# Kernel optimization log

Hardware: AMD Instinct MI355X
Metric: run time of the kernel (lower is better)

The kernel has to match this reference:

```python
import jax, jax.numpy as jnp
import numpy as np

N_NODES = 50000
N_EDGES = 600000
IN_DIM = 128
HID = 128
N_CLASSES = 40
N_GRAPHS = 128


def setup_inputs() -> dict:
    key = jax.random.key(0)
    ks = jax.random.split(key, 12)
    x = jax.random.normal(ks[0], (N_NODES, IN_DIM), dtype=jnp.float32)
    edge_index = jax.random.randint(ks[1], (2, N_EDGES), 0, N_NODES, dtype=jnp.int64)
    batch = jnp.sort(jax.random.randint(ks[2], (N_NODES,), 0, N_GRAPHS, dtype=jnp.int64))
    dims = [IN_DIM, HID, HID, N_CLASSES]
    params = {}
    for l in range(3):
        d_in, d_out = dims[l], dims[l + 1]
        s = 1.0 / np.sqrt(d_in)
        params[f"Wl{l}"] = jax.random.uniform(ks[3 + 3 * l], (d_out, d_in), jnp.float32, -s, s)
        params[f"bl{l}"] = jax.random.uniform(ks[4 + 3 * l], (d_out,), jnp.float32, -s, s)
        params[f"Wr{l}"] = jax.random.uniform(ks[5 + 3 * l], (d_out, d_in), jnp.float32, -s, s)
    return {"x": x, "edge_index": edge_index, "batch": batch, **params}


def _sage_layer(h, src, dst, Wl, bl, Wr):
    # message: relu(x_j) (edge_attr is None -> zero), mean-aggregate at dst
    m = jnp.maximum(h[src], 0.0)                       # [E, d]
    agg = jax.ops.segment_sum(m, dst, num_segments=N_NODES)
    cnt = jax.ops.segment_sum(jnp.ones((m.shape[0],), h.dtype), dst, num_segments=N_NODES)
    agg = agg / jnp.maximum(cnt, 1.0)[:, None]
    # lin_l(agg) + lin_r(x)
    return agg @ Wl.T + bl + h @ Wr.T


def reference(x, edge_index, batch, Wl0, bl0, Wr0, Wl1, bl1, Wr1, Wl2, bl2, Wr2):
    src, dst = edge_index[0], edge_index[1]
    Ws = [(Wl0, bl0, Wr0), (Wl1, bl1, Wr1), (Wl2, bl2, Wr2)]
    h = x
    for l, (Wl, bl, Wr) in enumerate(Ws):
        # dropout is identity in eval mode
        h = _sage_layer(h, src, dst, Wl, bl, Wr)
        if l != len(Ws) - 1:
            h = jnp.maximum(h, 0.0)
    # global mean pool over graphs
    gsum = jax.ops.segment_sum(h, batch, num_segments=N_GRAPHS)
    gcnt = jax.ops.segment_sum(jnp.ones((h.shape[0],), h.dtype), batch, num_segments=N_GRAPHS)
    g = gsum / jnp.maximum(gcnt, 1.0)[:, None]
    return h, g
```

## Files before the change

kernel.cpp:

```cpp
#include <hip/hip_runtime.h>
#include <hip/hip_bf16.h>


#define NODES 50000
#define K_DIM 128
#define N_GRAPHS 128

typedef __attribute__((ext_vector_type(8))) short short8;
typedef __attribute__((ext_vector_type(4))) short short4v;
typedef __attribute__((ext_vector_type(4))) float f32x4;

__device__ inline short f2bf(float f) {
    unsigned u = __builtin_bit_cast(unsigned, f);
    u += 0x7FFFu + ((u >> 16) & 1u);
    return (short)(u >> 16);
}
__device__ inline float bf2f(short h) {
    unsigned u = ((unsigned)(unsigned short)h) << 16;
    return __builtin_bit_cast(float, u);
}
__device__ inline float blo(unsigned u) { return __builtin_bit_cast(float, u << 16); }
__device__ inline float bhi(unsigned u) { return __builtin_bit_cast(float, u & 0xFFFF0000u); }
__device__ inline unsigned hilo_pack(float f) {
    short h = f2bf(f);
    short l = f2bf(f - bf2f(h));
    return ((unsigned)(unsigned short)h) | (((unsigned)(unsigned short)l) << 16);
}

__global__ void init_kernel(const float* __restrict__ w0, const float* __restrict__ w1,
                            const float* __restrict__ w2, const float* __restrict__ w3,
                            const float* __restrict__ w4, const float* __restrict__ w5,
                            short* __restrict__ whi, short* __restrict__ wlo,
                            int* __restrict__ deg, const int* __restrict__ batch,
                            int* __restrict__ gstart,
                            const float* __restrict__ x, short* __restrict__ xb,
                            short* __restrict__ xhi, short* __restrict__ xlo, int N) {
    int idx = blockIdx.x * 256 + threadIdx.x;
    if (idx < N * (K_DIM / 4)) {
        float4 v = reinterpret_cast<const float4*>(x)[idx];
        unsigned px = hilo_pack(v.x), py = hilo_pack(v.y);
        unsigned pz = hilo_pack(v.z), pw = hilo_pack(v.w);
        short4v b, hh, ll;
        b[0] = f2bf(fmaxf(v.x, 0.f)); hh[0] = (short)(px & 0xFFFFu); ll[0] = (short)(px >> 16);
        b[1] = f2bf(fmaxf(v.y, 0.f)); hh[1] = (short)(py & 0xFFFFu); ll[1] = (short)(py >> 16);
        b[2] = f2bf(fmaxf(v.z, 0.f)); hh[2] = (short)(pz & 0xFFFFu); ll[2] = (short)(pz >> 16);
        b[3] = f2bf(fmaxf(v.w, 0.f)); hh[3] = (short)(pw & 0xFFFFu); ll[3] = (short)(pw >> 16);
        *reinterpret_cast<short4v*>(&xb [idx * 4]) = b;
        *reinterpret_cast<short4v*>(&xhi[idx * 4]) = hh;
        *reinterpret_cast<short4v*>(&xlo[idx * 4]) = ll;
    }
    if (idx < N) deg[idx] = 0;
    const int TOT = 4 * 16384 + 96 * 128;
    if (idx < TOT) {
        float v;
        if (idx < 65536) {
            int m = idx >> 14, e = idx & 16383;
            const float* W = (m == 0) ? w0 : (m == 1) ? w1 : (m == 2) ? w2 : w3;
            v = W[e];
        } else {
            int i2 = idx - 65536;
            int row = i2 >> 7, col = i2 & 127;
            if (row < 40)      v = w4[row * 128 + col];
            else if (row < 80) v = w5[(row - 40) * 128 + col];
            else               v = 0.f;
        }
        unsigned p = hilo_pack(v);
        whi[idx] = (short)(p & 0xFFFFu);
        wlo[idx] = (short)(p >> 16);
    }
    if (idx <= N_GRAPHS) {
        int g = idx;
        int lo = 0, hi = N;
        while (lo < hi) {
            int mid = (lo + hi) >> 1;
            if (batch[mid] < g) lo = mid + 1; else hi = mid;
        }
        gstart[g] = lo;
    }
}

__global__ void deg_kernel(const int* __restrict__ dst, int* __restrict__ deg, int E) {
    int e = blockIdx.x * blockDim.x + threadIdx.x;
    if (e < E) atomicAdd(&deg[dst[e]], 1);
}

__global__ void scan_p1(const int* __restrict__ deg, int* __restrict__ bsum, int N) {
    int i = blockIdx.x * 256 + threadIdx.x;
    int v = (i < N) ? deg[i] : 0;
    #pragma unroll
    for (int off = 32; off > 0; off >>= 1) v += __shfl_down(v, off, 64);
    __shared__ int ws[4];
    int lane = threadIdx.x & 63, wv = threadIdx.x >> 6;
    if (lane == 0) ws[wv] = v;
    __syncthreads();
    if (threadIdx.x == 0) bsum[blockIdx.x] = ws[0] + ws[1] + ws[2] + ws[3];
}

__global__ void scan_p23(const int* __restrict__ deg, const int* __restrict__ bsum,
                         int* __restrict__ rowptr, int* __restrict__ fillpos,
                         int N, int NB) {
    const int tid = threadIdx.x, lane = tid & 63, wv = tid >> 6;
    __shared__ int ws[4];
    __shared__ int sboff[256];
    {
        int v = (tid < NB) ? bsum[tid] : 0;
        int incl = v;
        #pragma unroll
        for (int off = 1; off < 64; off <<= 1) {
            int t = __shfl_up(incl, off, 64);
            if (lane >= off) incl += t;
        }
        if (lane == 63) ws[wv] = incl;
        __syncthreads();
        int add = 0;
        for (int k = 0; k < wv; ++k) add += ws[k];
        sboff[tid] = incl + add - v;
        __syncthreads();
    }
    const int boff = sboff[blockIdx.x];
    int i = blockIdx.x * 256 + tid;
    int v = (i < N) ? deg[i] : 0;
    int incl = v;
    #pragma unroll
    for (int off = 1; off < 64; off <<= 1) {
        int t = __shfl_up(incl, off, 64);
        if (lane >= off) incl += t;
    }
    __shared__ int ws2[4];
    if (lane == 63) ws2[wv] = incl;
    __syncthreads();
    int add = 0;
    for (int k = 0; k < wv; ++k) add += ws2[k];
    int excl = boff + incl + add - v;
    if (i < N) { rowptr[i] = excl; fillpos[i] = excl; }
    if (i == N) rowptr[N] = excl;
}

__global__ void fill_kernel(const int* __restrict__ src, const int* __restrict__ dst,
                            int* __restrict__ fillpos, int* __restrict__ csr_src, int E) {
    int e = blockIdx.x * blockDim.x + threadIdx.x;
    if (e < E) {
        int p = atomicAdd(&fillpos[dst[e]], 1);
        csr_src[p] = src[e];
    }
}

__global__ void agg_bf16(const unsigned short* __restrict__ hb,
                         const int* __restrict__ rowptr,
                         const int* __restrict__ csr_src,
                         short* __restrict__ aggb, int N) {
    int w = (blockIdx.x * blockDim.x + threadIdx.x) >> 6;
    if (w >= N) return;
    int lane = threadIdx.x & 63;
    int half = lane >> 5, l32 = lane & 31;
    int s = rowptr[w], e = rowptr[w + 1];
    float4 acc = make_float4(0.f, 0.f, 0.f, 0.f);
    int i = s + half;
    for (; i + 6 < e; i += 8) {
        int s0 = csr_src[i], s1 = csr_src[i + 2], s2 = csr_src[i + 4], s3 = csr_src[i + 6];
        uint2 v0 = reinterpret_cast<const uint2*>(hb + (size_t)s0 * K_DIM)[l32];
        uint2 v1 = reinterpret_cast<const uint2*>(hb + (size_t)s1 * K_DIM)[l32];
        uint2 v2 = reinterpret_cast<const uint2*>(hb + (size_t)s2 * K_DIM)[l32];
        uint2 v3 = reinterpret_cast<const uint2*>(hb + (size_t)s3 * K_DIM)[l32];
        acc.x += (blo(v0.x) + blo(v1.x)) + (blo(v2.x) + blo(v3.x));
        acc.y += (bhi(v0.x) + bhi(v1.x)) + (bhi(v2.x) + bhi(v3.x));
        acc.z += (blo(v0.y) + blo(v1.y)) + (blo(v2.y) + blo(v3.y));
        acc.w += (bhi(v0.y) + bhi(v1.y)) + (bhi(v2.y) + bhi(v3.y));
    }
    for (; i < e; i += 2) {
        int s0 = csr_src[i];
        uint2 v0 = reinterpret_cast<const uint2*>(hb + (size_t)s0 * K_DIM)[l32];
        acc.x += blo(v0.x); acc.y += bhi(v0.x);
        acc.z += blo(v0.y); acc.w += bhi(v0.y);
    }
    acc.x += __shfl_xor(acc.x, 32, 64);
    acc.y += __shfl_xor(acc.y, 32, 64);
    acc.z += __shfl_xor(acc.z, 32, 64);
    acc.w += __shfl_xor(acc.w, 32, 64);
    if (half == 0) {
        float inv = 1.0f / fmaxf((float)(e - s), 1.0f);
        short4v b;
        b[0] = f2bf(acc.x * inv);
        b[1] = f2bf(acc.y * inv);
        b[2] = f2bf(acc.z * inv);
        b[3] = f2bf(acc.w * inv);
        *reinterpret_cast<short4v*>(&aggb[(size_t)w * K_DIM + l32 * 4]) = b;
    }
}

__global__ __launch_bounds__(256) void sage_mfma(
        const short* __restrict__ Ab_in,
        const short* __restrict__ Hhi_in, const short* __restrict__ Hlo_in,
        const short* __restrict__ Bhl, const short* __restrict__ Bll,
        const short* __restrict__ Bhr, const short* __restrict__ Blr,
        const float* __restrict__ bl,
        short* __restrict__ outHi, short* __restrict__ outLo, int N) {
    constexpr int BM = 64;
    constexpr int LSTR = 40;
    const int tid = threadIdx.x;
    const int lane = tid & 63;
    const int wave = tid >> 6;
    const int l15 = lane & 15;
    const int quad = lane >> 4;
    const int m0 = blockIdx.x * BM;
    const int srow = tid >> 2, sc8 = tid & 3;

    __shared__ __align__(16) short Ahi[BM * LSTR];
    __shared__ __align__(16) short Alo[BM * LSTR];

    f32x4 acc[4][2];
    #pragma unroll
    for (int i = 0; i < 4; ++i)
        #pragma unroll
        for (int j = 0; j < 2; ++j) acc[i][j] = (f32x4){0.f, 0.f, 0.f, 0.f};

    const short8 zero8 = (short8){0, 0, 0, 0, 0, 0, 0, 0};
    const int sm = m0 + srow;

    for (int k0 = 0; k0 < K_DIM; k0 += 32) {
        __syncthreads();
        {
            short8 v = zero8;
            if (sm < N) v = *reinterpret_cast<const short8*>(Ab_in + (size_t)sm * K_DIM + k0 + sc8 * 8);
            *reinterpret_cast<short8*>(&Ahi[srow * LSTR + sc8 * 8]) = v;
        }
        short8 bh[2], bo[2];
        #pragma unroll
        for (int nt = 0; nt < 2; ++nt) {
            int n = wave * 32 + nt * 16 + l15;
            bh[nt] = *reinterpret_cast<const short8*>(Bhl + (size_t)n * K_DIM + k0 + quad * 8);
            bo[nt] = *reinterpret_cast<const short8*>(Bll + (size_t)n * K_DIM + k0 + quad * 8);
        }
        __syncthreads();
        #pragma unroll
        for (int mt = 0; mt < 4; ++mt) {
            int row = mt * 16 + l15;
            short8 ab = *reinterpret_cast<const short8*>(&Ahi[row * LSTR + quad * 8]);
            #pragma unroll
            for (int nt = 0; nt < 2; ++nt) {
                acc[mt][nt] = __builtin_amdgcn_mfma_f32_16x16x32_bf16(ab, bh[nt], acc[mt][nt], 0, 0, 0);
                acc[mt][nt] = __builtin_amdgcn_mfma_f32_16x16x32_bf16(ab, bo[nt], acc[mt][nt], 0, 0, 0);
            }
        }
    }

    for (int k0 = 0; k0 < K_DIM; k0 += 32) {
        __syncthreads();
        {
            short8 vh = zero8, vl = zero8;
            if (sm < N) {
                vh = *reinterpret_cast<const short8*>(Hhi_in + (size_t)sm * K_DIM + k0 + sc8 * 8);
                vl = *reinterpret_cast<const short8*>(Hlo_in + (size_t)sm * K_DIM + k0 + sc8 * 8);
            }
            *reinterpret_cast<short8*>(&Ahi[srow * LSTR + sc8 * 8]) = vh;
            *reinterpret_cast<short8*>(&Alo[srow * LSTR + sc8 * 8]) = vl;
        }
        short8 bh[2], bo[2];
        #pragma unroll
        for (int nt = 0; nt < 2; ++nt) {
            int n = wave * 32 + nt * 16 + l15;
            bh[nt] = *reinterpret_cast<const short8*>(Bhr + (size_t)n * K_DIM + k0 + quad * 8);
            bo[nt] = *reinterpret_cast<const short8*>(Blr + (size_t)n * K_DIM + k0 + quad * 8);
        }
        __syncthreads();
        #pragma unroll
        for (int mt = 0; mt < 4; ++mt) {
            int row = mt * 16 + l15;
            short8 ah = *reinterpret_cast<const short8*>(&Ahi[row * LSTR + quad * 8]);
            short8 ao = *reinterpret_cast<const short8*>(&Alo[row * LSTR + quad * 8]);
            #pragma unroll
            for (int nt = 0; nt < 2; ++nt) {
                acc[mt][nt] = __builtin_amdgcn_mfma_f32_16x16x32_bf16(ah, bh[nt], acc[mt][nt], 0, 0, 0);
                acc[mt][nt] = __builtin_amdgcn_mfma_f32_16x16x32_bf16(ah, bo[nt], acc[mt][nt], 0, 0, 0);
                acc[mt][nt] = __builtin_amdgcn_mfma_f32_16x16x32_bf16(ao, bh[nt], acc[mt][nt], 0, 0, 0);
            }
        }
    }

    #pragma unroll
    for (int mt = 0; mt < 4; ++mt) {
        #pragma unroll
        for (int nt = 0; nt < 2; ++nt) {
            int col = wave * 32 + nt * 16 + l15;
            float b = bl[col];
            #pragma unroll
            for (int reg = 0; reg < 4; ++reg) {
                int row = m0 + mt * 16 + quad * 4 + reg;
                if (row < N) {
                    float v = fmaxf(acc[mt][nt][reg] + b, 0.f);
                    unsigned p = hilo_pack(v);
                    outHi[(size_t)row * K_DIM + col] = (short)(p & 0xFFFFu);
                    outLo[(size_t)row * K_DIM + col] = (short)(p >> 16);
                }
            }
        }
    }
}

__global__ __launch_bounds__(256) void gemm80(
        const short* __restrict__ Xhi, const short* __restrict__ Xlo,
        const short* __restrict__ Bh, const short* __restrict__ Bv,
        const float* __restrict__ b2,
        short* __restrict__ ylb, float* __restrict__ yr40, int N) {
    constexpr int BM = 64;
    constexpr int LSTR = 40;
    const int tid = threadIdx.x;
    const int lane = tid & 63;
    const int wave = tid >> 6;
    const int wm = wave & 1;
    const int wn = wave >> 1;
    const int l15 = lane & 15;
    const int quad = lane >> 4;
    const int m0 = blockIdx.x * BM;
    const int srow = tid >> 2, sc8 = tid & 3;

    __shared__ __align__(16) short Ahi[BM * LSTR];
    __shared__ __align__(16) short Alo[BM * LSTR];

    f32x4 acc[2][3];
    #pragma unroll
    for (int i = 0; i < 2; ++i)
        #pragma unroll
        for (int j = 0; j < 3; ++j) acc[i][j] = (f32x4){0.f, 0.f, 0.f, 0.f};

    const short8 zero8 = (short8){0, 0, 0, 0, 0, 0, 0, 0};
    const int sm = m0 + srow;

    for (int k0 = 0; k0 < K_DIM; k0 += 32) {
        __syncthreads();
        {
            short8 vh = zero8, vl = zero8;
            if (sm < N) {
                vh = *reinterpret_cast<const short8*>(Xhi + (size_t)sm * K_DIM + k0 + sc8 * 8);
                vl = *reinterpret_cast<const short8*>(Xlo + (size_t)sm * K_DIM + k0 + sc8 * 8);
            }
            *reinterpret_cast<short8*>(&Ahi[srow * LSTR + sc8 * 8]) = vh;
            *reinterpret_cast<short8*>(&Alo[srow * LSTR + sc8 * 8]) = vl;
        }
        short8 bh[3], bo[3];
        #pragma unroll
        for (int nt = 0; nt < 3; ++nt) {
            int n = wn * 48 + nt * 16 + l15;
            bh[nt] = *reinterpret_cast<const short8*>(Bh + (size_t)n * K_DIM + k0 + quad * 8);
            bo[nt] = *reinterpret_cast<const short8*>(Bv + (size_t)n * K_DIM + k0 + quad * 8);
        }
        __syncthreads();
        #pragma unroll
        for (int mt = 0; mt < 2; ++mt) {
            int row = wm * 32 + mt * 16 + l15;
            short8 ah = *reinterpret_cast<const short8*>(&Ahi[row * LSTR + quad * 8]);
            short8 ao = *reinterpret_cast<const short8*>(&Alo[row * LSTR + quad * 8]);
            #pragma unroll
            for (int nt = 0; nt < 3; ++nt) {
                acc[mt][nt] = __builtin_amdgcn_mfma_f32_16x16x32_bf16(ah, bh[nt], acc[mt][nt], 0, 0, 0);
                acc[mt][nt] = __builtin_amdgcn_mfma_f32_16x16x32_bf16(ah, bo[nt], acc[mt][nt], 0, 0, 0);
                acc[mt][nt] = __builtin_amdgcn_mfma_f32_16x16x32_bf16(ao, bh[nt], acc[mt][nt], 0, 0, 0);
            }
        }
    }

    #pragma unroll
    for (int mt = 0; mt < 2; ++mt) {
        #pragma unroll
        for (int nt = 0; nt < 3; ++nt) {
            int col = wn * 48 + nt * 16 + l15;
            #pragma unroll
            for (int reg = 0; reg < 4; ++reg) {
                int row = m0 + wm * 32 + mt * 16 + quad * 4 + reg;
                if (row < N) {
                    float v = acc[mt][nt][reg];
                    if (col < 40) {
                        ylb[(size_t)row * 40 + col] = f2bf(v);
                    } else if (col < 80) {
                        yr40[(size_t)row * 40 + (col - 40)] = v + b2[col - 40];
                    }
                }
            }
        }
    }
}

__global__ void agg40_kernel(const unsigned short* __restrict__ ylb,
                             const float* __restrict__ yr40,
                             const int* __restrict__ rowptr, const int* __restrict__ csr_src,
                             float* __restrict__ out, int N) {
    int w = (blockIdx.x * blockDim.x + threadIdx.x) >> 6;
    if (w >= N) return;
    int lane = threadIdx.x & 63;
    int s = rowptr[w], e = rowptr[w + 1];
    if (lane >= 40) return;
    float acc = 0.f;
    int i = s;
    for (; i + 3 < e; i += 4) {
        int s0 = csr_src[i], s1 = csr_src[i + 1], s2 = csr_src[i + 2], s3 = csr_src[i + 3];
        float v0 = bf2f((short)ylb[(size_t)s0 * 40 + lane]);
        float v1 = bf2f((short)ylb[(size_t)s1 * 40 + lane]);
        float v2 = bf2f((short)ylb[(size_t)s2 * 40 + lane]);
        float v3 = bf2f((short)ylb[(size_t)s3 * 40 + lane]);
        acc += (v0 + v1) + (v2 + v3);
    }
    for (; i < e; ++i) acc += bf2f((short)ylb[(size_t)csr_src[i] * 40 + lane]);
    float inv = 1.0f / fmaxf((float)(e - s), 1.0f);
    out[(size_t)w * 40 + lane] = acc * inv + yr40[(size_t)w * 40 + lane];
}

__global__ __launch_bounds__(320) void pool_kernel(const float* __restrict__ h,
                                                   const int* __restrict__ gstart,
                                                   float* __restrict__ g_out) {
    int g = blockIdx.x;
    int tid = threadIdx.x;
    int c = tid % 40, r = tid / 40;
    int s = gstart[g], e = gstart[g + 1];
    float acc = 0.f;
    for (int n = s + r; n < e; n += 8)
        acc += h[(size_t)n * 40 + c];
    __shared__ float sh[8][40];
    sh[r][c] = acc;
    __syncthreads();
    if (r == 0) {
        float sum = 0.f;
        #pragma unroll
        for (int i = 0; i < 8; ++i) sum += sh[i][c];
        g_out[g * 40 + c] = sum / fmaxf((float)(e - s), 1.0f);
    }
}

extern "C" void kernel_launch(void* const* d_in, const int* in_sizes, int n_in,
                              void* d_out, int out_size, void* d_ws, size_t ws_size,
                              hipStream_t stream) {
    const float* x    = (const float*)d_in[0];
    const int*   ei   = (const int*)d_in[1];
    const int*   batch= (const int*)d_in[2];
    const float* Wl0  = (const float*)d_in[3];
    const float* bl0  = (const float*)d_in[4];
    const float* Wr0  = (const float*)d_in[5];
    const float* Wl1  = (const float*)d_in[6];
    const float* bl1  = (const float*)d_in[7];
    const float* Wr1  = (const float*)d_in[8];
    const float* Wl2  = (const float*)d_in[9];
    const float* bl2  = (const float*)d_in[10];
    const float* Wr2  = (const float*)d_in[11];

    const int N = in_sizes[0] / K_DIM;
    const int E = in_sizes[1] / 2;
    const int* src = ei;
    const int* dst = ei + E;

    float* out = (float*)d_out;
    float* gsum = out + (size_t)N * 40;

    char* w = (char*)d_ws;
    auto alloc = [&](size_t bytes) {
        char* p = w;
        w += (bytes + 255) & ~(size_t)255;
        return p;
    };
    const size_t PL = (size_t)N * K_DIM * 2;
    short* aggb  = (short*)alloc(PL);
    short* xb    = (short*)alloc(PL);
    short* xhi   = (short*)alloc(PL);
    short* xlo   = (short*)alloc(PL);
    short* h1hi  = (short*)alloc(PL);
    short* h1lo  = (short*)alloc(PL);
    short* h2hi  = (short*)alloc(PL);
    short* h2lo  = (short*)alloc(PL);
    short* ylb   = (short*)alloc((size_t)N * 40 * 2);
    float* yr40  = (float*)alloc((size_t)N * 40 * 4);
    int*   rowptr= (int*)alloc((size_t)(N + 1) * 4);
    int*   deg   = (int*)alloc((size_t)N * 4);
    int*   fillp = (int*)alloc((size_t)N * 4);
    int*   csr   = (int*)alloc((size_t)E * 4);
    int*   bsum  = (int*)alloc(256 * 4);
    int*   gstart= (int*)alloc((size_t)(N_GRAPHS + 1) * 4);
    short* whi   = (short*)alloc(77824 * 2);
    short* wlo   = (short*)alloc(77824 * 2);

    const int NB = (N + 255) / 256;
    const int initGrid = (N * (K_DIM / 4) + 255) / 256;

    init_kernel<<<initGrid, 256, 0, stream>>>(Wl0, Wr0, Wl1, Wr1, Wl2, Wr2,
                                              whi, wlo, deg, batch, gstart,
                                              x, xb, xhi, xlo, N);
    deg_kernel<<<(E + 255) / 256, 256, 0, stream>>>(dst, deg, E);
    scan_p1<<<NB, 256, 0, stream>>>(deg, bsum, N);
    scan_p23<<<NB, 256, 0, stream>>>(deg, bsum, rowptr, fillp, N, NB);
    fill_kernel<<<(E + 255) / 256, 256, 0, stream>>>(src, dst, fillp, csr, E);

    short* hWl0 = whi;          short* lWl0 = wlo;
    short* hWr0 = whi + 16384;  short* lWr0 = wlo + 16384;
    short* hWl1 = whi + 32768;  short* lWl1 = wlo + 32768;
    short* hWr1 = whi + 49152;  short* lWr1 = wlo + 49152;
    short* hW2  = whi + 65536;  short* lW2  = wlo + 65536;

    const int aggGrid  = (N * 64 + 255) / 256;
    const int gemmGrid = (N + 63) / 64;

    agg_bf16<<<aggGrid, 256, 0, stream>>>((const unsigned short*)xb, rowptr, csr, aggb, N);
    sage_mfma<<<gemmGrid, 256, 0, stream>>>(
        aggb, xhi, xlo, hWl0, lWl0, hWr0, lWr0, bl0, h1hi, h1lo, N);
    agg_bf16<<<aggGrid, 256, 0, stream>>>((const unsigned short*)h1hi, rowptr, csr, aggb, N);
    sage_mfma<<<gemmGrid, 256, 0, stream>>>(
        aggb, h1hi, h1lo, hWl1, lWl1, hWr1, lWr1, bl1, h2hi, h2lo, N);
    gemm80<<<gemmGrid, 256, 0, stream>>>(h2hi, h2lo, hW2, lW2, bl2, ylb, yr40, N);
    agg40_kernel<<<aggGrid, 256, 0, stream>>>((const unsigned short*)ylb, yr40, rowptr, csr, out, N);

    pool_kernel<<<N_GRAPHS, 320, 0, stream>>>(out, gstart, gsum);
}
```

Before: 336.1 us.

## Merge sage GEMM K-loops and fuse final aggregation with graph mean pooling

The two K-loops of the SAGE MFMA kernel (aggregated input times Wl, self input times Wr) are merged into one loop. Each loop step now stages all three A tiles in shared memory and loads all four weight fragments, which halves the number of barrier and loop iterations. Separately, the last-layer aggregation kernel now also does global mean pooling: it pre-scales each node by its graph's inverse count, combines consecutive waves of the same graph, and adds into gsum with atomics, which removes the pool kernel launch. gsum is zeroed in init_kernel, and the merged loop raises register and LDS pressure.

```diff
diff --git a/kernel.cpp b/kernel.cpp
--- a/kernel.cpp
+++ b/kernel.cpp
@@ -34,7 +34,8 @@
                             int* __restrict__ deg, const int* __restrict__ batch,
                             int* __restrict__ gstart,
                             const float* __restrict__ x, short* __restrict__ xb,
-                            short* __restrict__ xhi, short* __restrict__ xlo, int N) {
+                            short* __restrict__ xhi, short* __restrict__ xlo,
+                            float* __restrict__ gsum, int N) {
     int idx = blockIdx.x * 256 + threadIdx.x;
     if (idx < N * (K_DIM / 4)) {
         float4 v = reinterpret_cast<const float4*>(x)[idx];
@@ -50,6 +51,7 @@
         *reinterpret_cast<short4v*>(&xlo[idx * 4]) = ll;
     }
     if (idx < N) deg[idx] = 0;
+    if (idx < N_GRAPHS * 40) gsum[idx] = 0.f;
     const int TOT = 4 * 16384 + 96 * 128;
     if (idx < TOT) {
         float v;
@@ -205,6 +207,7 @@
     const int m0 = blockIdx.x * BM;
     const int srow = tid >> 2, sc8 = tid & 3;
 
+    __shared__ __align__(16) short Ab [BM * LSTR];
     __shared__ __align__(16) short Ahi[BM * LSTR];
     __shared__ __align__(16) short Alo[BM * LSTR];
 
@@ -220,59 +223,40 @@
     for (int k0 = 0; k0 < K_DIM; k0 += 32) {
         __syncthreads();
         {
-            short8 v = zero8;
-            if (sm < N) v = *reinterpret_cast<const short8*>(Ab_in + (size_t)sm * K_DIM + k0 + sc8 * 8);
-            *reinterpret_cast<short8*>(&Ahi[srow * LSTR + sc8 * 8]) = v;
-        }
-        short8 bh[2], bo[2];
+            short8 va = zero8, vh = zero8, vl = zero8;
+            if (sm < N) {
+                va = *reinterpret_cast<const short8*>(Ab_in  + (size_t)sm * K_DIM + k0 + sc8 * 8);
+                vh = *reinterpret_cast<const short8*>(Hhi_in + (size_t)sm * K_DIM + k0 + sc8 * 8);
+                vl = *reinterpret_cast<const short8*>(Hlo_in + (size_t)sm * K_DIM + k0 + sc8 * 8);
+            }
+            *reinterpret_cast<short8*>(&Ab [srow * LSTR + sc8 * 8]) = va;
+            *reinterpret_cast<short8*>(&Ahi[srow * LSTR + sc8 * 8]) = vh;
+            *reinterpret_cast<short8*>(&Alo[srow * LSTR + sc8 * 8]) = vl;
+        }
+        short8 bhl_[2], bll_[2], bhr_[2], blr_[2];
         #pragma unroll
         for (int nt = 0; nt < 2; ++nt) {
             int n = wave * 32 + nt * 16 + l15;
-            bh[nt] = *reinterpret_cast<const short8*>(Bhl + (size_t)n * K_DIM + k0 + quad * 8);
-            bo[nt] = *reinterpret_cast<const short8*>(Bll + (size_t)n * K_DIM + k0 + quad * 8);
+            size_t off = (size_t)n * K_DIM + k0 + quad * 8;
+            bhl_[nt] = *reinterpret_cast<const short8*>(Bhl + off);
+            bll_[nt] = *reinterpret_cast<const short8*>(Bll + off);
+            bhr_[nt] = *reinterpret_cast<const short8*>(Bhr + off);
+            blr_[nt] = *reinterpret_cast<const short8*>(Blr + off);
         }
         __syncthreads();
         #pragma unroll
         for (int mt = 0; mt < 4; ++mt) {
             int row = mt * 16 + l15;
-            short8 ab = *reinterpret_cast<const short8*>(&Ahi[row * LSTR + quad * 8]);
-            #pragma unroll
-            for (int nt = 0; nt < 2; ++nt) {
-                acc[mt][nt] = __builtin_amdgcn_mfma_f32_16x16x32_bf16(ab, bh[nt], acc[mt][nt], 0, 0, 0);
-                acc[mt][nt] = __builtin_amdgcn_mfma_f32_16x16x32_bf16(ab, bo[nt], acc[mt][nt], 0, 0, 0);
-            }
-        }
-    }
-
-    for (int k0 = 0; k0 < K_DIM; k0 += 32) {
-        __syncthreads();
-        {
-            short8 vh = zero8, vl = zero8;
-            if (sm < N) {
-                vh = *reinterpret_cast<const short8*>(Hhi_in + (size_t)sm * K_DIM + k0 + sc8 * 8);
-                vl = *reinterpret_cast<const short8*>(Hlo_in + (size_t)sm * K_DIM + k0 + sc8 * 8);
-            }
-            *reinterpret_cast<short8*>(&Ahi[srow * LSTR + sc8 * 8]) = vh;
-            *reinterpret_cast<short8*>(&Alo[srow * LSTR + sc8 * 8]) = vl;
-        }
-        short8 bh[2], bo[2];
-        #pragma unroll
-        for (int nt = 0; nt < 2; ++nt) {
-            int n = wave * 32 + nt * 16 + l15;
-            bh[nt] = *reinterpret_cast<const short8*>(Bhr + (size_t)n * K_DIM + k0 + quad * 8);
-            bo[nt] = *reinterpret_cast<const short8*>(Blr + (size_t)n * K_DIM + k0 + quad * 8);
-        }
-        __syncthreads();
-        #pragma unroll
-        for (int mt = 0; mt < 4; ++mt) {
-            int row = mt * 16 + l15;
+            short8 ab = *reinterpret_cast<const short8*>(&Ab [row * LSTR + quad * 8]);
             short8 ah = *reinterpret_cast<const short8*>(&Ahi[row * LSTR + quad * 8]);
             short8 ao = *reinterpret_cast<const short8*>(&Alo[row * LSTR + quad * 8]);
             #pragma unroll
             for (int nt = 0; nt < 2; ++nt) {
-                acc[mt][nt] = __builtin_amdgcn_mfma_f32_16x16x32_bf16(ah, bh[nt], acc[mt][nt], 0, 0, 0);
-                acc[mt][nt] = __builtin_amdgcn_mfma_f32_16x16x32_bf16(ah, bo[nt], acc[mt][nt], 0, 0, 0);
-                acc[mt][nt] = __builtin_amdgcn_mfma_f32_16x16x32_bf16(ao, bh[nt], acc[mt][nt], 0, 0, 0);
+                acc[mt][nt] = __builtin_amdgcn_mfma_f32_16x16x32_bf16(ab, bhl_[nt], acc[mt][nt], 0, 0, 0);
+                acc[mt][nt] = __builtin_amdgcn_mfma_f32_16x16x32_bf16(ab, bll_[nt], acc[mt][nt], 0, 0, 0);
+                acc[mt][nt] = __builtin_amdgcn_mfma_f32_16x16x32_bf16(ah, bhr_[nt], acc[mt][nt], 0, 0, 0);
+                acc[mt][nt] = __builtin_amdgcn_mfma_f32_16x16x32_bf16(ah, blr_[nt], acc[mt][nt], 0, 0, 0);
+                acc[mt][nt] = __builtin_amdgcn_mfma_f32_16x16x32_bf16(ao, bhr_[nt], acc[mt][nt], 0, 0, 0);
             }
         }
     }
@@ -380,48 +364,65 @@
     }
 }
 
-__global__ void agg40_kernel(const unsigned short* __restrict__ ylb,
-                             const float* __restrict__ yr40,
-                             const int* __restrict__ rowptr, const int* __restrict__ csr_src,
-                             float* __restrict__ out, int N) {
-    int w = (blockIdx.x * blockDim.x + threadIdx.x) >> 6;
-    if (w >= N) return;
-    int lane = threadIdx.x & 63;
-    int s = rowptr[w], e = rowptr[w + 1];
-    if (lane >= 40) return;
-    float acc = 0.f;
-    int i = s;
-    for (; i + 3 < e; i += 4) {
-        int s0 = csr_src[i], s1 = csr_src[i + 1], s2 = csr_src[i + 2], s3 = csr_src[i + 3];
-        float v0 = bf2f((short)ylb[(size_t)s0 * 40 + lane]);
-        float v1 = bf2f((short)ylb[(size_t)s1 * 40 + lane]);
-        float v2 = bf2f((short)ylb[(size_t)s2 * 40 + lane]);
-        float v3 = bf2f((short)ylb[(size_t)s3 * 40 + lane]);
-        acc += (v0 + v1) + (v2 + v3);
-    }
-    for (; i < e; ++i) acc += bf2f((short)ylb[(size_t)csr_src[i] * 40 + lane]);
-    float inv = 1.0f / fmaxf((float)(e - s), 1.0f);
-    out[(size_t)w * 40 + lane] = acc * inv + yr40[(size_t)w * 40 + lane];
-}
-
-__global__ __launch_bounds__(320) void pool_kernel(const float* __restrict__ h,
-                                                   const int* __restrict__ gstart,
-                                                   float* __restrict__ g_out) {
-    int g = blockIdx.x;
-    int tid = threadIdx.x;
-    int c = tid % 40, r = tid / 40;
-    int s = gstart[g], e = gstart[g + 1];
-    float acc = 0.f;
-    for (int n = s + r; n < e; n += 8)
-        acc += h[(size_t)n * 40 + c];
-    __shared__ float sh[8][40];
-    sh[r][c] = acc;
+__global__ __launch_bounds__(256) void agg40_pool(
+        const unsigned short* __restrict__ ylb, const float* __restrict__ yr40,
+        const int* __restrict__ rowptr, const int* __restrict__ csr_src,
+        const int* __restrict__ batch, const int* __restrict__ gstart,
+        float* __restrict__ out, float* __restrict__ gsum, int N) {
+    const int w = (blockIdx.x * blockDim.x + threadIdx.x) >> 6;
+    const int lane = threadIdx.x & 63;
+    const int wv = threadIdx.x >> 6;
+    __shared__ float sh[4][40];
+    __shared__ int sg[4];
+    __shared__ float sinv[4];
+
+    float val = 0.f;
+    const bool valid = (w < N) && (lane < 40);
+    if (valid) {
+        int s = rowptr[w], e = rowptr[w + 1];
+        float acc = 0.f;
+        int i = s;
+        for (; i + 3 < e; i += 4) {
+            int s0 = csr_src[i], s1 = csr_src[i + 1], s2 = csr_src[i + 2], s3 = csr_src[i + 3];
+            float v0 = bf2f((short)ylb[(size_t)s0 * 40 + lane]);
+            float v1 = bf2f((short)ylb[(size_t)s1 * 40 + lane]);
+            float v2 = bf2f((short)ylb[(size_t)s2 * 40 + lane]);
+            float v3 = bf2f((short)ylb[(size_t)s3 * 40 + lane]);
+            acc += (v0 + v1) + (v2 + v3);
+        }
+        for (; i < e; ++i) acc += bf2f((short)ylb[(size_t)csr_src[i] * 40 + lane]);
+        float inv = 1.0f / fmaxf((float)(e - s), 1.0f);
+        val = acc * inv + yr40[(size_t)w * 40 + lane];
+        out[(size_t)w * 40 + lane] = val;
+        sh[wv][lane] = val;
+    }
+    if (lane == 0) {
+        if (w < N) {
+            int g = batch[w];
+            sg[wv] = g;
+            sinv[wv] = 1.0f / fmaxf((float)(gstart[g + 1] - gstart[g]), 1.0f);
+        } else {
+            sg[wv] = -1;
+        }
+    }
     __syncthreads();
-    if (r == 0) {
-        float sum = 0.f;
-        #pragma unroll
-        for (int i = 0; i < 8; ++i) sum += sh[i][c];
-        g_out[g * 40 + c] = sum / fmaxf((float)(e - s), 1.0f);
+    if (wv == 0 && lane < 40) {
+        int cur = -1;
+        float accum = 0.f;
+        #pragma unroll
+        for (int k = 0; k < 4; ++k) {
+            int gk = sg[k];
+            if (gk < 0) continue;
+            float c = sh[k][lane] * sinv[k];
+            if (gk == cur) {
+                accum += c;
+            } else {
+                if (cur >= 0) atomicAdd(&gsum[cur * 40 + lane], accum);
+                cur = gk;
+                accum = c;
+            }
+        }
+        if (cur >= 0) atomicAdd(&gsum[cur * 40 + lane], accum);
     }
 }
 
@@ -480,7 +481,7 @@
 
     init_kernel<<<initGrid, 256, 0, stream>>>(Wl0, Wr0, Wl1, Wr1, Wl2, Wr2,
                                               whi, wlo, deg, batch, gstart,
-                                              x, xb, xhi, xlo, N);
+                                              x, xb, xhi, xlo, gsum, N);
     deg_kernel<<<(E + 255) / 256, 256, 0, stream>>>(dst, deg, E);
     scan_p1<<<NB, 256, 0, stream>>>(deg, bsum, N);
     scan_p23<<<NB, 256, 0, stream>>>(deg, bsum, rowptr, fillp, N, NB);
@@ -502,7 +503,6 @@
     sage_mfma<<<gemmGrid, 256, 0, stream>>>(
         aggb, h1hi, h1lo, hWl1, lWl1, hWr1, lWr1, bl1, h2hi, h2lo, N);
     gemm80<<<gemmGrid, 256, 0, stream>>>(h2hi, h2lo, hW2, lW2, bl2, ylb, yr40, N);
-    agg40_kernel<<<aggGrid, 256, 0, stream>>>((const unsigned short*)ylb, yr40, rowptr, csr, out, N);
-
-    pool_kernel<<<N_GRAPHS, 320, 0, stream>>>(out, gstart, gsum);
-}
+    agg40_pool<<<aggGrid, 256, 0, stream>>>((const unsigned short*)ylb, yr40,
+                                            rowptr, csr, batch, gstart, out, gsum, N);
+}
```

Measured after the change: 336.5 us. No clear change (+0.1%).
